# Optimization experiments

Measured on AMD Instinct MI355X. Metric: run time of the kernel, lower is better.

The kernel has to match this reference:

```python
import jax, jax.numpy as jnp
import numpy as np

B, C, H, W = 8, 256, 64, 64
CQK = C // 8  # 32


def setup_inputs() -> dict:
    key = jax.random.key(0)
    ks = jax.random.split(key, 8)
    s = 0.05
    return {
        "x": jax.random.normal(ks[0], (B, C, H, W), dtype=jnp.float32),
        "wq": jax.random.normal(ks[1], (CQK, C), dtype=jnp.float32) * s,
        "bq": jax.random.normal(ks[2], (CQK,), dtype=jnp.float32) * s,
        "wk": jax.random.normal(ks[3], (CQK, C), dtype=jnp.float32) * s,
        "bk": jax.random.normal(ks[4], (CQK,), dtype=jnp.float32) * s,
        "wv": jax.random.normal(ks[5], (C, C), dtype=jnp.float32) * s,
        "bv": jax.random.normal(ks[6], (C,), dtype=jnp.float32) * s,
        "gamma": jax.random.normal(ks[7], (1,), dtype=jnp.float32),
    }


def reference(x, wq, bq, wk, bk, wv, bv, gamma):
    b, c, h, w = x.shape
    xf = x.reshape(b, c, h * w)  # [B, C, N]
    # conv1d kernel-size-1 == per-token linear over channels
    f = jnp.einsum('oc,bcn->bon', wq, xf) + bq[None, :, None]  # [B, C/8, N]
    g = jnp.einsum('oc,bcn->bon', wk, xf) + bk[None, :, None]  # [B, C/8, N]
    hh = jnp.einsum('oc,bcn->bon', wv, xf) + bv[None, :, None]  # [B, C, N]
    # scores[b, i, j] = sum_o f[b, o, i] * g[b, o, j]; NO 1/sqrt(d) scaling
    scores = jnp.einsum('boi,boj->bij', f, g)  # [B, N, N]
    # softmax over dim=1 (the f/query index axis), as in the original
    beta = jax.nn.softmax(scores, axis=1)
    # o[b, c, j] = gamma * sum_i hh[b, c, i] * beta[b, i, j] + xf
    o = gamma[0] * jnp.einsum('bci,bij->bcj', hh, beta) + xf
    return o.reshape(b, c, h, w)
```

## Files before the change

### kernel.cpp

```cpp
#include <hip/hip_runtime.h>
#include <stdint.h>

#define B_ 8
#define C_ 256
#define N_ 4096
#define LOG2E 1.44269504088896f
#define SHIFT 14.0f

typedef _Float16 half8 __attribute__((ext_vector_type(8)));
typedef _Float16 half4 __attribute__((ext_vector_type(4)));
typedef float floatx4 __attribute__((ext_vector_type(4)));

__global__ __launch_bounds__(256) void k_transpose(const float* __restrict__ x,
                                                   _Float16* __restrict__ xT) {
    __shared__ float tile[64][65];
    int i0 = blockIdx.x * 64;
    int c0 = blockIdx.y * 64;
    int b  = blockIdx.z;
    int t  = threadIdx.x;
    const float* xb = x + ((size_t)(b * C_ + c0)) * N_ + i0;
    int r4 = t >> 4;
    int c4 = (t & 15) * 4;
#pragma unroll
    for (int k = 0; k < 4; ++k) {
        int r = k * 16 + r4;
        *(float4*)&tile[r][c4] = *(const float4*)&xb[(size_t)r * N_ + c4];
    }
    __syncthreads();
    _Float16* xTb = xT + ((size_t)(b * N_ + i0)) * C_ + c0;
    int i2 = t >> 2;
#pragma unroll
    for (int g = 0; g < 2; ++g) {
        int ch = (t & 3) + g * 4;
        half8 v;
#pragma unroll
        for (int j = 0; j < 8; ++j) v[j] = (_Float16)tile[ch * 8 + j][i2];
        *(half8*)&xTb[(size_t)i2 * C_ + ch * 8] = v;
    }
}

__global__ __launch_bounds__(256) void k_wprep(const float* __restrict__ wq, const float* __restrict__ bq,
                                               const float* __restrict__ wk, const float* __restrict__ bk,
                                               const float* __restrict__ wv, const float* __restrict__ bv,
                                               _Float16* __restrict__ Whf, float* __restrict__ Bh) {
    int r = blockIdx.x;
    int t = threadIdx.x;
    const float* src;
    float bias;
    if (r < 32)      { src = wq + r * 256;        bias = bq[r]; }
    else if (r < 64) { src = wk + (r - 32) * 256; bias = bk[r - 32]; }
    else             { src = wv + (r - 64) * 256; bias = bv[r - 64]; }
    Whf[(t >> 3) * 2560 + r * 8 + (t & 7)] = (_Float16)src[t];
    if (t == 0) Bh[r] = bias;
}

__global__ __launch_bounds__(256) void k_proj(const _Float16* __restrict__ xT,
                                              const _Float16* __restrict__ Whf,
                                              const float* __restrict__ Bh,
                                              _Float16* __restrict__ Kf,
                                              _Float16* __restrict__ Qf,
                                              _Float16* __restrict__ Vf) {
    __shared__ _Float16 As[64 * 264] __attribute__((aligned(16)));
    int id = blockIdx.x;
    int b  = id & 7;
    int i0 = (id >> 3) * 64;
    int t = threadIdx.x;
    int w = t >> 6, lane = t & 63, col = lane & 15, q = lane >> 4;
    const _Float16* xTb = xT + ((size_t)(b * N_ + i0)) * 256;
#pragma unroll
    for (int rep = 0; rep < 8; ++rep) {
        int idx = t + rep * 256;
        int i = idx >> 5, part = idx & 31;
        *(uint4*)&As[i * 264 + part * 8] = *(const uint4*)&xTb[(size_t)i * 256 + part * 8];
    }
    __syncthreads();
    floatx4 acc[4][5];
#pragma unroll
    for (int mt = 0; mt < 4; ++mt)
#pragma unroll
        for (int nt = 0; nt < 5; ++nt) acc[mt][nt] = (floatx4){0.f, 0.f, 0.f, 0.f};
    for (int kc = 0; kc < 8; ++kc) {
        half8 a[4], bf[5];
#pragma unroll
        for (int nt = 0; nt < 5; ++nt)
            bf[nt] = *(const half8*)&Whf[(kc * 4 + q) * 2560 + (w * 80 + nt * 16 + col) * 8];
#pragma unroll
        for (int mt = 0; mt < 4; ++mt)
            a[mt] = *(const half8*)&As[(mt * 16 + col) * 264 + kc * 32 + q * 8];
#pragma unroll
        for (int mt = 0; mt < 4; ++mt)
#pragma unroll
            for (int nt = 0; nt < 5; ++nt)
                acc[mt][nt] = __builtin_amdgcn_mfma_f32_16x16x32_f16(a[mt], bf[nt], acc[mt][nt], 0, 0, 0);
    }
#pragma unroll
    for (int nt = 0; nt < 5; ++nt) {
        int n = w * 80 + nt * 16 + col;
        float bias = Bh[n];
        if (n < 32) {
#pragma unroll
            for (int mt = 0; mt < 4; ++mt)
#pragma unroll
                for (int r = 0; r < 4; ++r) {
                    int i = i0 + mt * 16 + q * 4 + r;
                    Kf[((((size_t)b * 128 + (i >> 5)) * 4 + (n >> 3)) * 32 + (i & 31)) * 8 + (n & 7)]
                        = (_Float16)(acc[mt][nt][r] + bias);
                }
        } else if (n < 64) {
            int n2 = n - 32;
#pragma unroll
            for (int mt = 0; mt < 4; ++mt)
#pragma unroll
                for (int r = 0; r < 4; ++r) {
                    int j = i0 + mt * 16 + q * 4 + r;
                    Qf[((((size_t)b * 128 + (j >> 5)) * 4 + (n2 >> 3)) * 32 + (j & 31)) * 8 + (n2 & 7)]
                        = (_Float16)(acc[mt][nt][r] + bias);
                }
        } else {
            int c = n - 64;
#pragma unroll
            for (int mt = 0; mt < 4; ++mt) {
                int ib = (i0 >> 4) + mt;
                half4 v4;
#pragma unroll
                for (int r = 0; r < 4; ++r) v4[r] = (_Float16)(acc[mt][nt][r] + bias);
                *(half4*)&Vf[(((size_t)b * 256 + ib) * 256 + c) * 16 + q * 4] = v4;
            }
        }
    }
}

__global__ __launch_bounds__(512, 4) void k_attn(const _Float16* __restrict__ Kf,
                                                 const _Float16* __restrict__ Qf,
                                                 const _Float16* __restrict__ Vf,
                                                 const float* __restrict__ x,
                                                 const float* __restrict__ gptr,
                                                 float* __restrict__ out) {
    __shared__ _Float16 Ps[2][64 * 72] __attribute__((aligned(16)));
    __shared__ float Lp[2][64];
    int id = blockIdx.x;
    int b  = id & 7;
    int j0 = (id >> 3) * 64;
    int t = threadIdx.x;
    int w = t >> 6, lane = t & 63, col = lane & 15, q = lane >> 4;
    int jts = w & 3, ihs = w >> 2;
    int cw  = w * 32;
    const _Float16* Kfb = Kf + (size_t)b * 131072;
    const _Float16* Qfb = Qf + (size_t)b * 131072;
    const _Float16* Vfb = Vf + (size_t)b * 1048576;
    int jj = j0 + jts * 16;
    half8 bq = *(const half8*)&Qfb[((((jj >> 5)) * 4 + q) * 32 + ((jj & 31) + col)) * 8];
    floatx4 acc[2][4];
#pragma unroll
    for (int ct = 0; ct < 2; ++ct)
#pragma unroll
        for (int jt = 0; jt < 4; ++jt) acc[ct][jt] = (floatx4){0.f, 0.f, 0.f, 0.f};
    float lacc = 0.f;
    {
        half8 aK0[2];
#pragma unroll
        for (int itl = 0; itl < 2; ++itl)
            aK0[itl] = *(const half8*)&Kfb[((((size_t)0 * 2 + ihs) * 4 + q) * 32 + itl * 16 + col) * 8];
#pragma unroll
        for (int itl = 0; itl < 2; ++itl) {
            floatx4 s = __builtin_amdgcn_mfma_f32_16x16x32_f16(aK0[itl], bq,
                                                               (floatx4){0.f, 0.f, 0.f, 0.f}, 0, 0, 0);
            half4 ph;
#pragma unroll
            for (int r = 0; r < 4; ++r) {
                float p = exp2f((s[r] - SHIFT) * LOG2E);
                lacc += p;
                ph[r] = (_Float16)p;
            }
            *(half4*)&Ps[0][(jts * 16 + col) * 72 + ihs * 32 + itl * 16 + q * 4] = ph;
        }
    }
    __syncthreads();
    for (int it = 0; it < 64; ++it) {
        const _Float16* cur = Ps[it & 1];
        _Float16* nxt = Ps[(it + 1) & 1];
        half8 vA[4];
#pragma unroll
        for (int kk = 0; kk < 2; ++kk)
#pragma unroll
            for (int ct = 0; ct < 2; ++ct)
                vA[ct * 2 + kk] = *(const half8*)&Vfb[
                    (((size_t)(it * 4 + kk * 2 + (q >> 1))) * 256 + cw + ct * 16 + col) * 16 + (q & 1) * 8];
        half8 aKr[2];
        if (it < 63) {
#pragma unroll
            for (int itl = 0; itl < 2; ++itl)
                aKr[itl] = *(const half8*)&Kfb[((((it + 1) * 2 + ihs) * 4 + q) * 32 + itl * 16 + col) * 8];
        }
#pragma unroll
        for (int kk = 0; kk < 2; ++kk) {
            half8 bfr[4];
#pragma unroll
            for (int jt = 0; jt < 4; ++jt)
                bfr[jt] = *(const half8*)&cur[(jt * 16 + col) * 72 + kk * 32 + q * 8];
#pragma unroll
            for (int ct = 0; ct < 2; ++ct)
#pragma unroll
                for (int jt = 0; jt < 4; ++jt)
                    acc[ct][jt] = __builtin_amdgcn_mfma_f32_16x16x32_f16(vA[ct * 2 + kk], bfr[jt], acc[ct][jt], 0, 0, 0);
        }
        if (it < 63) {
#pragma unroll
            for (int itl = 0; itl < 2; ++itl) {
                floatx4 s = __builtin_amdgcn_mfma_f32_16x16x32_f16(aKr[itl], bq,
                                                                   (floatx4){0.f, 0.f, 0.f, 0.f}, 0, 0, 0);
                half4 ph;
#pragma unroll
                for (int r = 0; r < 4; ++r) {
                    float p = exp2f((s[r] - SHIFT) * LOG2E);
                    lacc += p;
                    ph[r] = (_Float16)p;
                }
                *(half4*)&nxt[(jts * 16 + col) * 72 + ihs * 32 + itl * 16 + q * 4] = ph;
            }
        }
        __syncthreads();
    }
    lacc += __shfl_xor(lacc, 16, 64);
    lacc += __shfl_xor(lacc, 32, 64);
    if (lane < 16) Lp[ihs][jts * 16 + lane] = lacc;
    __syncthreads();
    float gamma = gptr[0];
    const float* xb = x + (size_t)b * C_ * N_;
    float* ob = out + (size_t)b * C_ * N_;
#pragma unroll
    for (int jt = 0; jt < 4; ++jt) {
        int jl = jt * 16 + col;
        float li = 1.0f / (Lp[0][jl] + Lp[1][jl]);
        int j = j0 + jl;
#pragma unroll
        for (int ct = 0; ct < 2; ++ct)
#pragma unroll
            for (int r = 0; r < 4; ++r) {
                int c = cw + ct * 16 + q * 4 + r;
                size_t off = (size_t)c * N_ + j;
                ob[off] = gamma * acc[ct][jt][r] * li + xb[off];
            }
    }
}

extern "C" void kernel_launch(void* const* d_in, const int* in_sizes, int n_in,
                              void* d_out, int out_size, void* d_ws, size_t ws_size,
                              hipStream_t stream) {
    const float* x  = (const float*)d_in[0];
    const float* wq = (const float*)d_in[1];
    const float* bq = (const float*)d_in[2];
    const float* wk = (const float*)d_in[3];
    const float* bk = (const float*)d_in[4];
    const float* wv = (const float*)d_in[5];
    const float* bv = (const float*)d_in[6];
    const float* gm = (const float*)d_in[7];
    float* out = (float*)d_out;
    char* ws = (char*)d_ws;
    _Float16* xT  = (_Float16*)ws;
    _Float16* Vf  = (_Float16*)(ws + 16777216);
    _Float16* Kf  = (_Float16*)(ws + 33554432);
    _Float16* Qf  = (_Float16*)(ws + 35651584);
    _Float16* Whf = (_Float16*)(ws + 37748736);
    float*    Bh  = (float*)(ws + 37912576);

    k_transpose<<<dim3(64, 4, 8), 256, 0, stream>>>(x, xT);
    k_wprep<<<dim3(320), 256, 0, stream>>>(wq, bq, wk, bk, wv, bv, Whf, Bh);
    k_proj<<<dim3(512), 256, 0, stream>>>(xT, Whf, Bh, Kf, Qf, Vf);
    k_attn<<<dim3(512), 512, 0, stream>>>(Kf, Qf, Vf, x, gm, out);
}
```

Before: 205.8 us.

## Fuse transpose into projection and software-pipeline V/K loads in attention

Removes the separate transpose kernel: the projection kernel now reads fp32 x directly, transposes it through a shared-memory tile and converts it to fp16 in-block. This drops the xT round trip through global memory and one kernel launch. The attention loop is unrolled by two, with V and K fragments prefetched one iteration ahead into alternating registers, pointer increments replacing index math, and the exp argument folded into a single FMA. The cost is more register pressure and extra shared memory and barriers in the projection kernel.

```diff
diff --git a/kernel.cpp b/kernel.cpp
--- a/kernel.cpp
+++ b/kernel.cpp
@@ -5,39 +5,11 @@
 #define C_ 256
 #define N_ 4096
 #define LOG2E 1.44269504088896f
-#define SHIFT 14.0f
+#define NSHIFT_L2E (-14.0f * 1.44269504088896f)
 
 typedef _Float16 half8 __attribute__((ext_vector_type(8)));
 typedef _Float16 half4 __attribute__((ext_vector_type(4)));
 typedef float floatx4 __attribute__((ext_vector_type(4)));
-
-__global__ __launch_bounds__(256) void k_transpose(const float* __restrict__ x,
-                                                   _Float16* __restrict__ xT) {
-    __shared__ float tile[64][65];
-    int i0 = blockIdx.x * 64;
-    int c0 = blockIdx.y * 64;
-    int b  = blockIdx.z;
-    int t  = threadIdx.x;
-    const float* xb = x + ((size_t)(b * C_ + c0)) * N_ + i0;
-    int r4 = t >> 4;
-    int c4 = (t & 15) * 4;
-#pragma unroll
-    for (int k = 0; k < 4; ++k) {
-        int r = k * 16 + r4;
-        *(float4*)&tile[r][c4] = *(const float4*)&xb[(size_t)r * N_ + c4];
-    }
-    __syncthreads();
-    _Float16* xTb = xT + ((size_t)(b * N_ + i0)) * C_ + c0;
-    int i2 = t >> 2;
-#pragma unroll
-    for (int g = 0; g < 2; ++g) {
-        int ch = (t & 3) + g * 4;
-        half8 v;
-#pragma unroll
-        for (int j = 0; j < 8; ++j) v[j] = (_Float16)tile[ch * 8 + j][i2];
-        *(half8*)&xTb[(size_t)i2 * C_ + ch * 8] = v;
-    }
-}
 
 __global__ __launch_bounds__(256) void k_wprep(const float* __restrict__ wq, const float* __restrict__ bq,
                                                const float* __restrict__ wk, const float* __restrict__ bk,
@@ -54,26 +26,39 @@
     if (t == 0) Bh[r] = bias;
 }
 
-__global__ __launch_bounds__(256) void k_proj(const _Float16* __restrict__ xT,
+__global__ __launch_bounds__(256) void k_proj(const float* __restrict__ x,
                                               const _Float16* __restrict__ Whf,
                                               const float* __restrict__ Bh,
                                               _Float16* __restrict__ Kf,
                                               _Float16* __restrict__ Qf,
                                               _Float16* __restrict__ Vf) {
+    __shared__ float xtile[64 * 65];
     __shared__ _Float16 As[64 * 264] __attribute__((aligned(16)));
     int id = blockIdx.x;
     int b  = id & 7;
     int i0 = (id >> 3) * 64;
     int t = threadIdx.x;
     int w = t >> 6, lane = t & 63, col = lane & 15, q = lane >> 4;
-    const _Float16* xTb = xT + ((size_t)(b * N_ + i0)) * 256;
-#pragma unroll
-    for (int rep = 0; rep < 8; ++rep) {
-        int idx = t + rep * 256;
-        int i = idx >> 5, part = idx & 31;
-        *(uint4*)&As[i * 264 + part * 8] = *(const uint4*)&xTb[(size_t)i * 256 + part * 8];
-    }
-    __syncthreads();
+    const float* xb = x + (size_t)b * C_ * N_ + i0;
+    for (int cc = 0; cc < 4; ++cc) {
+        int cr = t >> 4;
+        int ip = (t & 15) * 4;
+#pragma unroll
+        for (int k = 0; k < 4; ++k)
+            *(float4*)&xtile[(cr + 16 * k) * 65 + ip] =
+                *(const float4*)&xb[(size_t)(cc * 64 + cr + 16 * k) * N_ + ip];
+        __syncthreads();
+        int i = t & 63, cb2 = (t >> 6) * 16;
+        float v[16];
+#pragma unroll
+        for (int k = 0; k < 16; ++k) v[k] = xtile[(cb2 + k) * 65 + i];
+        half8 h0, h1;
+#pragma unroll
+        for (int k = 0; k < 8; ++k) { h0[k] = (_Float16)v[k]; h1[k] = (_Float16)v[8 + k]; }
+        *(half8*)&As[i * 264 + cc * 64 + cb2] = h0;
+        *(half8*)&As[i * 264 + cc * 64 + cb2 + 8] = h1;
+        __syncthreads();
+    }
     floatx4 acc[4][5];
 #pragma unroll
     for (int mt = 0; mt < 4; ++mt)
@@ -130,13 +115,60 @@
     }
 }
 
+#define PS_BUF 4608
+
+#define ATTN_STEP(IT, VCUR, VNXT, ROFF, WOFF)                                     \
+    {                                                                             \
+        if ((IT) < 63) {                                                          \
+            _Pragma("unroll")                                                     \
+            for (int ct = 0; ct < 2; ++ct) {                                      \
+                VNXT[ct * 2 + 0] = *(const half8*)(pV0 + ct * 256);               \
+                VNXT[ct * 2 + 1] = *(const half8*)(pV1 + ct * 256);               \
+            }                                                                     \
+            pV0 += 16384; pV1 += 16384;                                           \
+            aKn0 = *(const half8*)(pK);                                           \
+            aKn1 = *(const half8*)(pK + 128);                                     \
+            pK += 2048;                                                           \
+        }                                                                         \
+        _Pragma("unroll")                                                         \
+        for (int kk = 0; kk < 2; ++kk) {                                          \
+            half8 bfr[4];                                                         \
+            _Pragma("unroll")                                                     \
+            for (int jt = 0; jt < 4; ++jt)                                        \
+                bfr[jt] = *(const half8*)&PsF[psr + (ROFF) + jt * 1152 + kk * 32];\
+            _Pragma("unroll")                                                     \
+            for (int ct = 0; ct < 2; ++ct)                                        \
+                _Pragma("unroll")                                                 \
+                for (int jt = 0; jt < 4; ++jt)                                    \
+                    acc[ct][jt] = __builtin_amdgcn_mfma_f32_16x16x32_f16(         \
+                        VCUR[ct * 2 + kk], bfr[jt], acc[ct][jt], 0, 0, 0);        \
+        }                                                                         \
+        if ((IT) < 63) {                                                          \
+            _Pragma("unroll")                                                     \
+            for (int itl = 0; itl < 2; ++itl) {                                   \
+                floatx4 s = __builtin_amdgcn_mfma_f32_16x16x32_f16(               \
+                    itl ? aKn1 : aKn0, bq, (floatx4){0.f, 0.f, 0.f, 0.f}, 0, 0, 0);\
+                float p0 = exp2f(s[0] * LOG2E + NSHIFT_L2E);                      \
+                float p1 = exp2f(s[1] * LOG2E + NSHIFT_L2E);                      \
+                float p2 = exp2f(s[2] * LOG2E + NSHIFT_L2E);                      \
+                float p3 = exp2f(s[3] * LOG2E + NSHIFT_L2E);                      \
+                lacc += (p0 + p1) + (p2 + p3);                                    \
+                half4 ph;                                                         \
+                ph[0] = (_Float16)p0; ph[1] = (_Float16)p1;                       \
+                ph[2] = (_Float16)p2; ph[3] = (_Float16)p3;                       \
+                *(half4*)&PsF[psw + (WOFF) + itl * 16] = ph;                      \
+            }                                                                     \
+        }                                                                         \
+        __syncthreads();                                                          \
+    }
+
 __global__ __launch_bounds__(512, 4) void k_attn(const _Float16* __restrict__ Kf,
                                                  const _Float16* __restrict__ Qf,
                                                  const _Float16* __restrict__ Vf,
                                                  const float* __restrict__ x,
                                                  const float* __restrict__ gptr,
                                                  float* __restrict__ out) {
-    __shared__ _Float16 Ps[2][64 * 72] __attribute__((aligned(16)));
+    __shared__ _Float16 PsF[2 * PS_BUF] __attribute__((aligned(16)));
     __shared__ float Lp[2][64];
     int id = blockIdx.x;
     int b  = id & 7;
@@ -148,78 +180,48 @@
     const _Float16* Kfb = Kf + (size_t)b * 131072;
     const _Float16* Qfb = Qf + (size_t)b * 131072;
     const _Float16* Vfb = Vf + (size_t)b * 1048576;
-    int jj = j0 + jts * 16;
-    half8 bq = *(const half8*)&Qfb[((((jj >> 5)) * 4 + q) * 32 + ((jj & 31) + col)) * 8];
+    const _Float16* pK  = Kfb + ((ihs * 4 + q) * 32 + col) * 8;
+    const _Float16* pV0 = Vfb + ((q >> 1) * 256 + cw + col) * 16 + (q & 1) * 8;
+    const _Float16* pV1 = pV0 + 8192;
+    const int psw = (jts * 16 + col) * 72 + ihs * 32 + q * 4;
+    const int psr = col * 72 + q * 8;
     floatx4 acc[2][4];
 #pragma unroll
     for (int ct = 0; ct < 2; ++ct)
 #pragma unroll
         for (int jt = 0; jt < 4; ++jt) acc[ct][jt] = (floatx4){0.f, 0.f, 0.f, 0.f};
     float lacc = 0.f;
-    {
-        half8 aK0[2];
-#pragma unroll
-        for (int itl = 0; itl < 2; ++itl)
-            aK0[itl] = *(const half8*)&Kfb[((((size_t)0 * 2 + ihs) * 4 + q) * 32 + itl * 16 + col) * 8];
-#pragma unroll
-        for (int itl = 0; itl < 2; ++itl) {
-            floatx4 s = __builtin_amdgcn_mfma_f32_16x16x32_f16(aK0[itl], bq,
-                                                               (floatx4){0.f, 0.f, 0.f, 0.f}, 0, 0, 0);
-            half4 ph;
-#pragma unroll
-            for (int r = 0; r < 4; ++r) {
-                float p = exp2f((s[r] - SHIFT) * LOG2E);
-                lacc += p;
-                ph[r] = (_Float16)p;
-            }
-            *(half4*)&Ps[0][(jts * 16 + col) * 72 + ihs * 32 + itl * 16 + q * 4] = ph;
-        }
+    half8 vA[4], vB[4], aKn0, aKn1;
+#pragma unroll
+    for (int ct = 0; ct < 2; ++ct) {
+        vA[ct * 2 + 0] = *(const half8*)(pV0 + ct * 256);
+        vA[ct * 2 + 1] = *(const half8*)(pV1 + ct * 256);
+    }
+    pV0 += 16384; pV1 += 16384;
+    aKn0 = *(const half8*)(pK);
+    aKn1 = *(const half8*)(pK + 128);
+    pK += 2048;
+    int jj = j0 + jts * 16;
+    half8 bq = *(const half8*)&Qfb[(((jj >> 5) * 4 + q) * 32 + ((jj & 31) + col)) * 8];
+#pragma unroll
+    for (int itl = 0; itl < 2; ++itl) {
+        floatx4 s = __builtin_amdgcn_mfma_f32_16x16x32_f16(itl ? aKn1 : aKn0, bq,
+                                                           (floatx4){0.f, 0.f, 0.f, 0.f}, 0, 0, 0);
+        float p0 = exp2f(s[0] * LOG2E + NSHIFT_L2E);
+        float p1 = exp2f(s[1] * LOG2E + NSHIFT_L2E);
+        float p2 = exp2f(s[2] * LOG2E + NSHIFT_L2E);
+        float p3 = exp2f(s[3] * LOG2E + NSHIFT_L2E);
+        lacc += (p0 + p1) + (p2 + p3);
+        half4 ph;
+        ph[0] = (_Float16)p0; ph[1] = (_Float16)p1;
+        ph[2] = (_Float16)p2; ph[3] = (_Float16)p3;
+        *(half4*)&PsF[psw + itl * 16] = ph;
     }
     __syncthreads();
-    for (int it = 0; it < 64; ++it) {
-        const _Float16* cur = Ps[it & 1];
-        _Float16* nxt = Ps[(it + 1) & 1];
-        half8 vA[4];
-#pragma unroll
-        for (int kk = 0; kk < 2; ++kk)
-#pragma unroll
-            for (int ct = 0; ct < 2; ++ct)
-                vA[ct * 2 + kk] = *(const half8*)&Vfb[
-                    (((size_t)(it * 4 + kk * 2 + (q >> 1))) * 256 + cw + ct * 16 + col) * 16 + (q & 1) * 8];
-        half8 aKr[2];
-        if (it < 63) {
-#pragma unroll
-            for (int itl = 0; itl < 2; ++itl)
-                aKr[itl] = *(const half8*)&Kfb[((((it + 1) * 2 + ihs) * 4 + q) * 32 + itl * 16 + col) * 8];
-        }
-#pragma unroll
-        for (int kk = 0; kk < 2; ++kk) {
-            half8 bfr[4];
-#pragma unroll
-            for (int jt = 0; jt < 4; ++jt)
-                bfr[jt] = *(const half8*)&cur[(jt * 16 + col) * 72 + kk * 32 + q * 8];
-#pragma unroll
-            for (int ct = 0; ct < 2; ++ct)
-#pragma unroll
-                for (int jt = 0; jt < 4; ++jt)
-                    acc[ct][jt] = __builtin_amdgcn_mfma_f32_16x16x32_f16(vA[ct * 2 + kk], bfr[jt], acc[ct][jt], 0, 0, 0);
-        }
-        if (it < 63) {
-#pragma unroll
-            for (int itl = 0; itl < 2; ++itl) {
-                floatx4 s = __builtin_amdgcn_mfma_f32_16x16x32_f16(aKr[itl], bq,
-                                                                   (floatx4){0.f, 0.f, 0.f, 0.f}, 0, 0, 0);
-                half4 ph;
-#pragma unroll
-                for (int r = 0; r < 4; ++r) {
-                    float p = exp2f((s[r] - SHIFT) * LOG2E);
-                    lacc += p;
-                    ph[r] = (_Float16)p;
-                }
-                *(half4*)&nxt[(jts * 16 + col) * 72 + ihs * 32 + itl * 16 + q * 4] = ph;
-            }
-        }
-        __syncthreads();
+    for (int m = 0; m < 32; ++m) {
+        int it = m * 2;
+        ATTN_STEP(it,     vA, vB, 0,      PS_BUF)
+        ATTN_STEP(it + 1, vB, vA, PS_BUF, 0)
     }
     lacc += __shfl_xor(lacc, 16, 64);
     lacc += __shfl_xor(lacc, 32, 64);
@@ -257,15 +259,13 @@
     const float* gm = (const float*)d_in[7];
     float* out = (float*)d_out;
     char* ws = (char*)d_ws;
-    _Float16* xT  = (_Float16*)ws;
-    _Float16* Vf  = (_Float16*)(ws + 16777216);
-    _Float16* Kf  = (_Float16*)(ws + 33554432);
-    _Float16* Qf  = (_Float16*)(ws + 35651584);
-    _Float16* Whf = (_Float16*)(ws + 37748736);
-    float*    Bh  = (float*)(ws + 37912576);
-
-    k_transpose<<<dim3(64, 4, 8), 256, 0, stream>>>(x, xT);
+    _Float16* Vf  = (_Float16*)ws;
+    _Float16* Kf  = (_Float16*)(ws + 16777216);
+    _Float16* Qf  = (_Float16*)(ws + 18874368);
+    _Float16* Whf = (_Float16*)(ws + 20971520);
+    float*    Bh  = (float*)(ws + 21135360);
+
     k_wprep<<<dim3(320), 256, 0, stream>>>(wq, bq, wk, bk, wv, bv, Whf, Bh);
-    k_proj<<<dim3(512), 256, 0, stream>>>(xT, Whf, Bh, Kf, Qf, Vf);
+    k_proj<<<dim3(512), 256, 0, stream>>>(x, Whf, Bh, Kf, Qf, Vf);
     k_attn<<<dim3(512), 512, 0, stream>>>(Kf, Qf, Vf, x, gm, out);
 }
```

Measured after the change: 188.5 us. 8.4% less time.
